# Kernel tuning notes

Measured on AMD Instinct MI355X. Metric: run time of the kernel, lower is better.

Reference implementation:

```python
import jax, jax.numpy as jnp
import numpy as np

B, T, I, H, O = 8192, 512, 4, 32, 4


def setup_inputs() -> dict:
    key = jax.random.key(0)
    ks = jax.random.split(key, 11)
    s = 1.0 / np.sqrt(H)  # PyTorch RNN init scale
    return {
        "X": jax.random.normal(ks[0], (B, T, I), dtype=jnp.float32),
        "W_ih0": jax.random.uniform(ks[1], (H, I), minval=-s, maxval=s, dtype=jnp.float32),
        "W_hh0": jax.random.uniform(ks[2], (H, H), minval=-s, maxval=s, dtype=jnp.float32),
        "b_ih0": jax.random.uniform(ks[3], (H,), minval=-s, maxval=s, dtype=jnp.float32),
        "b_hh0": jax.random.uniform(ks[4], (H,), minval=-s, maxval=s, dtype=jnp.float32),
        "W_ih1": jax.random.uniform(ks[5], (H, H), minval=-s, maxval=s, dtype=jnp.float32),
        "W_hh1": jax.random.uniform(ks[6], (H, H), minval=-s, maxval=s, dtype=jnp.float32),
        "b_ih1": jax.random.uniform(ks[7], (H,), minval=-s, maxval=s, dtype=jnp.float32),
        "b_hh1": jax.random.uniform(ks[8], (H,), minval=-s, maxval=s, dtype=jnp.float32),
        "W_ll": jax.random.uniform(ks[9], (O, H), minval=-s, maxval=s, dtype=jnp.float32),
        "b_ll": jax.random.uniform(ks[10], (O,), minval=-s, maxval=s, dtype=jnp.float32),
    }


def reference(X, W_ih0, W_hh0, b_ih0, b_hh0, W_ih1, W_hh1, b_ih1, b_hh1, W_ll, b_ll):
    # 2-layer tanh RNN (batch_first), zero initial hidden state, then Linear head.
    b0 = b_ih0 + b_hh0
    b1 = b_ih1 + b_hh1
    Bsz = X.shape[0]
    Hdim = W_hh0.shape[0]
    h_init = (jnp.zeros((Bsz, Hdim), X.dtype), jnp.zeros((Bsz, Hdim), X.dtype))

    def step(h, x_t):
        h0, h1 = h
        h0 = jnp.tanh(x_t @ W_ih0.T + h0 @ W_hh0.T + b0)
        h1 = jnp.tanh(h0 @ W_ih1.T + h1 @ W_hh1.T + b1)
        return (h0, h1), h1

    xs = jnp.swapaxes(X, 0, 1)  # [T, B, I]
    _, ys = jax.lax.scan(step, h_init, xs)  # ys: [T, B, H]
    out = ys @ W_ll.T + b_ll  # [T, B, O]
    out = jnp.swapaxes(out, 0, 1)  # [B, T, O]
    return out.reshape(out.shape[0], -1)  # [B, T*O]
```

## Files before the change

### kernel.cpp

```cpp
#include <hip/hip_runtime.h>
#include <cstddef>
#include <cstdint>

constexpr int kB = 8192, kT = 512, kI = 4, kH = 32, kO = 4;

typedef _Float16 f16x8 __attribute__((ext_vector_type(8)));
typedef float    f32x4 __attribute__((ext_vector_type(4)));

#define MFMA(a, b, c) __builtin_amdgcn_mfma_f32_16x16x32_f16((a), (b), (c), 0, 0, 0)

__device__ __forceinline__ void bar_lds() {
    asm volatile("s_waitcnt lgkmcnt(0)" ::: "memory");
    __builtin_amdgcn_s_barrier();
    __builtin_amdgcn_sched_barrier(0);
}

__device__ __forceinline__ float fast_tanh(float x) {
    float e = __builtin_amdgcn_exp2f(x * 2.8853900817779268f);
    return 1.0f - 2.0f * __builtin_amdgcn_rcpf(e + 1.0f);
}

__device__ __forceinline__ float4 ld4(const float* p) { return *(const float4*)p; }

__device__ __forceinline__ f16x8 pack_frag(float4 lo, float4 hi) {
    f16x8 r;
    r[0] = (_Float16)lo.x; r[1] = (_Float16)lo.y;
    r[2] = (_Float16)lo.z; r[3] = (_Float16)lo.w;
    r[4] = (_Float16)hi.x; r[5] = (_Float16)hi.y;
    r[6] = (_Float16)hi.z; r[7] = (_Float16)hi.w;
    return r;
}

__device__ __forceinline__ f16x8 pack_state(f32x4 a, f32x4 b) {
    union { f16x8 v; uint32_t u[4]; } r;
    r.u[0] = __builtin_bit_cast(uint32_t, __builtin_amdgcn_cvt_pkrtz(a[0], a[1]));
    r.u[1] = __builtin_bit_cast(uint32_t, __builtin_amdgcn_cvt_pkrtz(a[2], a[3]));
    r.u[2] = __builtin_bit_cast(uint32_t, __builtin_amdgcn_cvt_pkrtz(b[0], b[1]));
    r.u[3] = __builtin_bit_cast(uint32_t, __builtin_amdgcn_cvt_pkrtz(b[2], b[3]));
    return r.v;
}

__device__ __forceinline__ f16x8 bxpack(float4 xn, bool g0) {
    union { f16x8 v; uint32_t u[4]; } bx;
    bx.u[0] = g0 ? __builtin_bit_cast(uint32_t, __builtin_amdgcn_cvt_pkrtz(xn.x, xn.y)) : 0u;
    bx.u[1] = g0 ? __builtin_bit_cast(uint32_t, __builtin_amdgcn_cvt_pkrtz(xn.z, xn.w)) : 0u;
    bx.u[2] = 0u; bx.u[3] = 0u;
    return bx.v;
}

__global__ __launch_bounds__(256, 2) void rnn2_roles(
    const float* __restrict__ X,
    const float* __restrict__ W_ih0, const float* __restrict__ W_hh0,
    const float* __restrict__ b_ih0, const float* __restrict__ b_hh0,
    const float* __restrict__ W_ih1, const float* __restrict__ W_hh1,
    const float* __restrict__ b_ih1, const float* __restrict__ b_hh1,
    const float* __restrict__ W_ll, const float* __restrict__ b_ll,
    float* __restrict__ out)
{
    const int  tid = threadIdx.x;
    const int  wid = tid >> 6;
    const int  l   = tid & 63;
    const int  c   = l & 15;
    const int  g   = l >> 4;
    const bool g0  = (g == 0);
    const int  b   = blockIdx.x * 16 + c;
    const int  k0  = 4 * g;
    const int  role = wid ^ (((blockIdx.x >> 3) & 1) << 1);

    __shared__ f32x4 xcring[2][2][64];
    __shared__ uint4 h0ring[2][64];
    __shared__ uint4 h1ring[2][64];

    const float4 z4 = make_float4(0.f, 0.f, 0.f, 0.f);
    union { f16x8 v; uint32_t u[4]; } zz;
    zz.u[0] = zz.u[1] = zz.u[2] = zz.u[3] = 0u;

    if (role == 0) {
        const float* wp = W_hh0 + c * kH;
        const f16x8 A0 = pack_frag(ld4(wp + k0), ld4(wp + 16 + k0));
        wp = W_hh0 + (c + 16) * kH;
        const f16x8 A1 = pack_frag(ld4(wp + k0), ld4(wp + 16 + k0));
        f16x8 Bh0 = zz.v;
        f32x4 xcR0 = {0.f,0.f,0.f,0.f}, xcR1 = {0.f,0.f,0.f,0.f};

        for (int pb = 0; pb < 130; ++pb) {
#pragma unroll
            for (int u = 0; u < 4; ++u) {
                const int p = pb * 4 + u;
                f32x4 nx0, nx1;
                const bool rd = (p >= 1) & (p <= 512);
                const bool go = (p >= 2) & (p <= 513);
                if (rd) {
                    nx0 = xcring[(p - 1) & 1][0][l];
                    nx1 = xcring[(p - 1) & 1][1][l];
                }
                if (go) {
                    f32x4 a0 = MFMA(A0, Bh0, xcR0);
                    f32x4 a1 = MFMA(A1, Bh0, xcR1);
                    f32x4 t0, t1;
#pragma unroll
                    for (int r = 0; r < 4; ++r) { t0[r] = fast_tanh(a0[r]); t1[r] = fast_tanh(a1[r]); }
                    Bh0 = pack_state(t0, t1);
                    h0ring[p & 1][l] = __builtin_bit_cast(uint4, Bh0);
                }
                if (rd) { xcR0 = nx0; xcR1 = nx1; }
                bar_lds();
            }
        }
    } else if (role == 1) {
        const float* wp = W_ih1 + c * kH;
        const f16x8 I0 = pack_frag(ld4(wp + k0), ld4(wp + 16 + k0));
        wp = W_ih1 + (c + 16) * kH;
        const f16x8 I1 = pack_frag(ld4(wp + k0), ld4(wp + 16 + k0));
        wp = W_hh1 + c * kH;
        const f16x8 H0w = pack_frag(ld4(wp + k0), ld4(wp + 16 + k0));
        wp = W_hh1 + (c + 16) * kH;
        const f16x8 H1w = pack_frag(ld4(wp + k0), ld4(wp + 16 + k0));
        f32x4 bias1_0, bias1_1;
#pragma unroll
        for (int r = 0; r < 4; ++r) {
            bias1_0[r] = b_ih1[k0 + r]      + b_hh1[k0 + r];
            bias1_1[r] = b_ih1[16 + k0 + r] + b_hh1[16 + k0 + r];
        }
        f16x8 Bh1 = zz.v;
        f32x4 pB0 = {0.f,0.f,0.f,0.f}, pB1 = {0.f,0.f,0.f,0.f};

        for (int pb = 0; pb < 130; ++pb) {
#pragma unroll
            for (int u = 0; u < 4; ++u) {
                const int p = pb * 4 + u;
                f16x8 H;
                const bool rd = (p >= 3) & (p <= 514);
                const bool go = (p >= 4) & (p <= 515);
                if (rd) H = __builtin_bit_cast(f16x8, h0ring[(p - 3) & 1][l]);
                if (go) {
                    f32x4 q0 = MFMA(H0w, Bh1, pB0);
                    f32x4 q1 = MFMA(H1w, Bh1, pB1);
                    f32x4 t0, t1;
#pragma unroll
                    for (int r = 0; r < 4; ++r) { t0[r] = fast_tanh(q0[r]); t1[r] = fast_tanh(q1[r]); }
                    Bh1 = pack_state(t0, t1);
                    h1ring[p & 1][l] = __builtin_bit_cast(uint4, Bh1);
                }
                if (rd) {
                    pB0 = MFMA(I0, H, bias1_0);
                    pB1 = MFMA(I1, H, bias1_1);
                }
                bar_lds();
            }
        }
    } else if (role == 2) {
        const f16x8 W0 = pack_frag(g0 ? ld4(W_ih0 + c * kI) : z4, z4);
        const f16x8 W1 = pack_frag(g0 ? ld4(W_ih0 + (c + 16) * kI) : z4, z4);
        f32x4 bias0_0, bias0_1;
#pragma unroll
        for (int r = 0; r < 4; ++r) {
            bias0_0[r] = b_ih0[k0 + r]      + b_hh0[k0 + r];
            bias0_1[r] = b_ih0[16 + k0 + r] + b_hh0[16 + k0 + r];
        }
        const float* xp = X + (size_t)b * (kT * kI);
        float4 xbuf[4];
#pragma unroll
        for (int u = 0; u < 4; ++u) xbuf[u] = ld4(xp + u * kI);

        for (int pb = 0; pb < 130; ++pb) {
#pragma unroll
            for (int u = 0; u < 4; ++u) {
                const int p = pb * 4 + u;
                if (p < kT) {
                    f16x8 bx = bxpack(xbuf[u], g0);
                    f32x4 c0 = MFMA(W0, bx, bias0_0);
                    f32x4 c1 = MFMA(W1, bx, bias0_1);
                    xcring[p & 1][0][l] = c0;
                    xcring[p & 1][1][l] = c1;
                    int idx = p + 4; idx = idx < kT ? idx : (kT - 1);
                    xbuf[u] = ld4(xp + idx * kI);
                }
                bar_lds();
            }
        }
    } else {
        const f16x8 All = (c < kO)
            ? pack_frag(ld4(W_ll + c * kH + k0), ld4(W_ll + c * kH + 16 + k0))
            : pack_frag(z4, z4);
        f32x4 biasll;
#pragma unroll
        for (int r = 0; r < 4; ++r) biasll[r] = g0 ? b_ll[r] : 0.f;
        float* op = out + (size_t)b * (kT * kO);

        for (int pb = 0; pb < 130; ++pb) {
#pragma unroll
            for (int u = 0; u < 4; ++u) {
                const int p = pb * 4 + u;
                const bool go = (p >= 5) & (p <= 516);
                if (go) {
                    f16x8 H1 = __builtin_bit_cast(f16x8, h1ring[(p - 1) & 1][l]);
                    f32x4 o = MFMA(All, H1, biasll);
                    if (g0) *(float4*)(op + (size_t)(p - 5) * kO) =
                        make_float4(o[0], o[1], o[2], o[3]);
                }
                bar_lds();
            }
        }
    }
}

extern "C" void kernel_launch(void* const* d_in, const int* in_sizes, int n_in,
                              void* d_out, int out_size, void* d_ws, size_t ws_size,
                              hipStream_t stream) {
    const float* X     = (const float*)d_in[0];
    const float* W_ih0 = (const float*)d_in[1];
    const float* W_hh0 = (const float*)d_in[2];
    const float* b_ih0 = (const float*)d_in[3];
    const float* b_hh0 = (const float*)d_in[4];
    const float* W_ih1 = (const float*)d_in[5];
    const float* W_hh1 = (const float*)d_in[6];
    const float* b_ih1 = (const float*)d_in[7];
    const float* b_hh1 = (const float*)d_in[8];
    const float* W_ll  = (const float*)d_in[9];
    const float* b_ll  = (const float*)d_in[10];
    float* out = (float*)d_out;

    rnn2_roles<<<dim3(kB / 16), dim3(256), 0, stream>>>(
        X, W_ih0, W_hh0, b_ih0, b_hh0, W_ih1, W_hh1, b_ih1, b_hh1, W_ll, b_ll, out);
}
```

Baseline: 148.8 us.

## Prescale RNN weights for exp2 tanh and peel role loops with 4-deep rings

Folds the 2/ln2 factor of the exp2-based tanh into the layer weights and biases at load time. This removes one multiply per tanh on the serial recurrence, and the final step becomes an fma. Each role's time loop is split into an unrolled prologue, a predicate-free steady-state loop and an unrolled epilogue. The LDS rings grow from 2 to 4 slots, and the role-to-wave swizzle now alternates per block. The per-step barrier is kept, so the gains come from shorter dependent chains and less predication. The cost is slightly more LDS and code size, plus the rounding error of scaling weights before the fp16 conversion.

```diff
diff --git a/kernel.cpp b/kernel.cpp
--- a/kernel.cpp
+++ b/kernel.cpp
@@ -8,6 +8,8 @@
 typedef float    f32x4 __attribute__((ext_vector_type(4)));
 
 #define MFMA(a, b, c) __builtin_amdgcn_mfma_f32_16x16x32_f16((a), (b), (c), 0, 0, 0)
+
+constexpr float kPre = 2.8853900817779268f;
 
 __device__ __forceinline__ void bar_lds() {
     asm volatile("s_waitcnt lgkmcnt(0)" ::: "memory");
@@ -15,12 +17,16 @@
     __builtin_amdgcn_sched_barrier(0);
 }
 
-__device__ __forceinline__ float fast_tanh(float x) {
-    float e = __builtin_amdgcn_exp2f(x * 2.8853900817779268f);
-    return 1.0f - 2.0f * __builtin_amdgcn_rcpf(e + 1.0f);
+__device__ __forceinline__ float fast_tanh_pre(float xp) {
+    float e = __builtin_amdgcn_exp2f(xp);
+    return fmaf(-2.0f, __builtin_amdgcn_rcpf(e + 1.0f), 1.0f);
 }
 
 __device__ __forceinline__ float4 ld4(const float* p) { return *(const float4*)p; }
+
+__device__ __forceinline__ float4 scl4(float4 v, float s) {
+    return make_float4(v.x * s, v.y * s, v.z * s, v.w * s);
+}
 
 __device__ __forceinline__ f16x8 pack_frag(float4 lo, float4 hi) {
     f16x8 r;
@@ -40,15 +46,15 @@
     return r.v;
 }
 
-__device__ __forceinline__ f16x8 bxpack(float4 xn, bool g0) {
+__device__ __forceinline__ f16x8 bxpack(float4 xn) {
     union { f16x8 v; uint32_t u[4]; } bx;
-    bx.u[0] = g0 ? __builtin_bit_cast(uint32_t, __builtin_amdgcn_cvt_pkrtz(xn.x, xn.y)) : 0u;
-    bx.u[1] = g0 ? __builtin_bit_cast(uint32_t, __builtin_amdgcn_cvt_pkrtz(xn.z, xn.w)) : 0u;
+    bx.u[0] = __builtin_bit_cast(uint32_t, __builtin_amdgcn_cvt_pkrtz(xn.x, xn.y));
+    bx.u[1] = __builtin_bit_cast(uint32_t, __builtin_amdgcn_cvt_pkrtz(xn.z, xn.w));
     bx.u[2] = 0u; bx.u[3] = 0u;
     return bx.v;
 }
 
-__global__ __launch_bounds__(256, 2) void rnn2_roles(
+__global__ __launch_bounds__(256, 2) void rnn2_pipe4(
     const float* __restrict__ X,
     const float* __restrict__ W_ih0, const float* __restrict__ W_hh0,
     const float* __restrict__ b_ih0, const float* __restrict__ b_hh0,
@@ -65,11 +71,11 @@
     const bool g0  = (g == 0);
     const int  b   = blockIdx.x * 16 + c;
     const int  k0  = 4 * g;
-    const int  role = wid ^ (((blockIdx.x >> 3) & 1) << 1);
-
-    __shared__ f32x4 xcring[2][2][64];
-    __shared__ uint4 h0ring[2][64];
-    __shared__ uint4 h1ring[2][64];
+    const int  role = wid ^ ((blockIdx.x & 1) << 1);
+
+    __shared__ f32x4 xcring[4][2][64];
+    __shared__ uint4 h0ring[4][64];
+    __shared__ uint4 h1ring[4][64];
 
     const float4 z4 = make_float4(0.f, 0.f, 0.f, 0.f);
     union { f16x8 v; uint32_t u[4]; } zz;
@@ -77,108 +83,116 @@
 
     if (role == 0) {
         const float* wp = W_hh0 + c * kH;
-        const f16x8 A0 = pack_frag(ld4(wp + k0), ld4(wp + 16 + k0));
+        const f16x8 A0w = pack_frag(scl4(ld4(wp + k0), kPre), scl4(ld4(wp + 16 + k0), kPre));
         wp = W_hh0 + (c + 16) * kH;
-        const f16x8 A1 = pack_frag(ld4(wp + k0), ld4(wp + 16 + k0));
+        const f16x8 A1w = pack_frag(scl4(ld4(wp + k0), kPre), scl4(ld4(wp + 16 + k0), kPre));
         f16x8 Bh0 = zz.v;
         f32x4 xcR0 = {0.f,0.f,0.f,0.f}, xcR1 = {0.f,0.f,0.f,0.f};
 
-        for (int pb = 0; pb < 130; ++pb) {
-#pragma unroll
-            for (int u = 0; u < 4; ++u) {
-                const int p = pb * 4 + u;
-                f32x4 nx0, nx1;
-                const bool rd = (p >= 1) & (p <= 512);
-                const bool go = (p >= 2) & (p <= 513);
-                if (rd) {
-                    nx0 = xcring[(p - 1) & 1][0][l];
-                    nx1 = xcring[(p - 1) & 1][1][l];
-                }
-                if (go) {
-                    f32x4 a0 = MFMA(A0, Bh0, xcR0);
-                    f32x4 a1 = MFMA(A1, Bh0, xcR1);
-                    f32x4 t0, t1;
-#pragma unroll
-                    for (int r = 0; r < 4; ++r) { t0[r] = fast_tanh(a0[r]); t1[r] = fast_tanh(a1[r]); }
-                    Bh0 = pack_state(t0, t1);
-                    h0ring[p & 1][l] = __builtin_bit_cast(uint4, Bh0);
-                }
-                if (rd) { xcR0 = nx0; xcR1 = nx1; }
-                bar_lds();
-            }
-        }
+        auto ph = [&](int p, bool rd, bool go) {
+            f32x4 nx0, nx1;
+            if (rd) {
+                nx0 = xcring[(p - 1) & 3][0][l];
+                nx1 = xcring[(p - 1) & 3][1][l];
+            }
+            if (go) {
+                f32x4 a0 = MFMA(A0w, Bh0, xcR0);
+                f32x4 a1 = MFMA(A1w, Bh0, xcR1);
+                f32x4 t0, t1;
+#pragma unroll
+                for (int r = 0; r < 4; ++r) { t0[r] = fast_tanh_pre(a0[r]); t1[r] = fast_tanh_pre(a1[r]); }
+                Bh0 = pack_state(t0, t1);
+                h0ring[(p - 2) & 3][l] = __builtin_bit_cast(uint4, Bh0);
+            }
+            if (rd) { xcR0 = nx0; xcR1 = nx1; }
+        };
+
+#pragma unroll
+        for (int p = 0; p < 8; ++p) { ph(p, p >= 1, p >= 2); bar_lds(); }
+        for (int pb = 0; pb < 124; ++pb) {
+#pragma unroll
+            for (int u = 0; u < 4; ++u) { ph(8 + pb * 4 + u, true, true); bar_lds(); }
+        }
+#pragma unroll
+        for (int p = 504; p < 520; ++p) { ph(p, p <= 512, p <= 513); bar_lds(); }
     } else if (role == 1) {
         const float* wp = W_ih1 + c * kH;
-        const f16x8 I0 = pack_frag(ld4(wp + k0), ld4(wp + 16 + k0));
+        const f16x8 I0 = pack_frag(scl4(ld4(wp + k0), kPre), scl4(ld4(wp + 16 + k0), kPre));
         wp = W_ih1 + (c + 16) * kH;
-        const f16x8 I1 = pack_frag(ld4(wp + k0), ld4(wp + 16 + k0));
+        const f16x8 I1 = pack_frag(scl4(ld4(wp + k0), kPre), scl4(ld4(wp + 16 + k0), kPre));
         wp = W_hh1 + c * kH;
-        const f16x8 H0w = pack_frag(ld4(wp + k0), ld4(wp + 16 + k0));
+        const f16x8 H0w = pack_frag(scl4(ld4(wp + k0), kPre), scl4(ld4(wp + 16 + k0), kPre));
         wp = W_hh1 + (c + 16) * kH;
-        const f16x8 H1w = pack_frag(ld4(wp + k0), ld4(wp + 16 + k0));
+        const f16x8 H1w = pack_frag(scl4(ld4(wp + k0), kPre), scl4(ld4(wp + 16 + k0), kPre));
         f32x4 bias1_0, bias1_1;
 #pragma unroll
         for (int r = 0; r < 4; ++r) {
-            bias1_0[r] = b_ih1[k0 + r]      + b_hh1[k0 + r];
-            bias1_1[r] = b_ih1[16 + k0 + r] + b_hh1[16 + k0 + r];
+            bias1_0[r] = (b_ih1[k0 + r]      + b_hh1[k0 + r])      * kPre;
+            bias1_1[r] = (b_ih1[16 + k0 + r] + b_hh1[16 + k0 + r]) * kPre;
         }
         f16x8 Bh1 = zz.v;
         f32x4 pB0 = {0.f,0.f,0.f,0.f}, pB1 = {0.f,0.f,0.f,0.f};
 
-        for (int pb = 0; pb < 130; ++pb) {
-#pragma unroll
-            for (int u = 0; u < 4; ++u) {
-                const int p = pb * 4 + u;
-                f16x8 H;
-                const bool rd = (p >= 3) & (p <= 514);
-                const bool go = (p >= 4) & (p <= 515);
-                if (rd) H = __builtin_bit_cast(f16x8, h0ring[(p - 3) & 1][l]);
-                if (go) {
-                    f32x4 q0 = MFMA(H0w, Bh1, pB0);
-                    f32x4 q1 = MFMA(H1w, Bh1, pB1);
-                    f32x4 t0, t1;
-#pragma unroll
-                    for (int r = 0; r < 4; ++r) { t0[r] = fast_tanh(q0[r]); t1[r] = fast_tanh(q1[r]); }
-                    Bh1 = pack_state(t0, t1);
-                    h1ring[p & 1][l] = __builtin_bit_cast(uint4, Bh1);
-                }
-                if (rd) {
-                    pB0 = MFMA(I0, H, bias1_0);
-                    pB1 = MFMA(I1, H, bias1_1);
-                }
-                bar_lds();
-            }
-        }
+        auto ph = [&](int p, bool rd, bool go) {
+            f16x8 Hn;
+            if (rd) Hn = __builtin_bit_cast(f16x8, h0ring[(p - 3) & 3][l]);
+            if (go) {
+                f32x4 q0 = MFMA(H0w, Bh1, pB0);
+                f32x4 q1 = MFMA(H1w, Bh1, pB1);
+                f32x4 t0, t1;
+#pragma unroll
+                for (int r = 0; r < 4; ++r) { t0[r] = fast_tanh_pre(q0[r]); t1[r] = fast_tanh_pre(q1[r]); }
+                Bh1 = pack_state(t0, t1);
+                h1ring[(p - 4) & 3][l] = __builtin_bit_cast(uint4, Bh1);
+            }
+            if (rd) {
+                pB0 = MFMA(I0, Hn, bias1_0);
+                pB1 = MFMA(I1, Hn, bias1_1);
+            }
+        };
+
+#pragma unroll
+        for (int p = 0; p < 8; ++p) { ph(p, p >= 3, p >= 4); bar_lds(); }
+        for (int pb = 0; pb < 124; ++pb) {
+#pragma unroll
+            for (int u = 0; u < 4; ++u) { ph(8 + pb * 4 + u, true, true); bar_lds(); }
+        }
+#pragma unroll
+        for (int p = 504; p < 520; ++p) { ph(p, p <= 514, p <= 515); bar_lds(); }
     } else if (role == 2) {
-        const f16x8 W0 = pack_frag(g0 ? ld4(W_ih0 + c * kI) : z4, z4);
-        const f16x8 W1 = pack_frag(g0 ? ld4(W_ih0 + (c + 16) * kI) : z4, z4);
+        const f16x8 W0 = pack_frag(g0 ? scl4(ld4(W_ih0 + c * kI), kPre) : z4, z4);
+        const f16x8 W1 = pack_frag(g0 ? scl4(ld4(W_ih0 + (c + 16) * kI), kPre) : z4, z4);
         f32x4 bias0_0, bias0_1;
 #pragma unroll
         for (int r = 0; r < 4; ++r) {
-            bias0_0[r] = b_ih0[k0 + r]      + b_hh0[k0 + r];
-            bias0_1[r] = b_ih0[16 + k0 + r] + b_hh0[16 + k0 + r];
+            bias0_0[r] = (b_ih0[k0 + r]      + b_hh0[k0 + r])      * kPre;
+            bias0_1[r] = (b_ih0[16 + k0 + r] + b_hh0[16 + k0 + r]) * kPre;
         }
         const float* xp = X + (size_t)b * (kT * kI);
         float4 xbuf[4];
 #pragma unroll
         for (int u = 0; u < 4; ++u) xbuf[u] = ld4(xp + u * kI);
 
-        for (int pb = 0; pb < 130; ++pb) {
-#pragma unroll
-            for (int u = 0; u < 4; ++u) {
-                const int p = pb * 4 + u;
-                if (p < kT) {
-                    f16x8 bx = bxpack(xbuf[u], g0);
-                    f32x4 c0 = MFMA(W0, bx, bias0_0);
-                    f32x4 c1 = MFMA(W1, bx, bias0_1);
-                    xcring[p & 1][0][l] = c0;
-                    xcring[p & 1][1][l] = c1;
-                    int idx = p + 4; idx = idx < kT ? idx : (kT - 1);
-                    xbuf[u] = ld4(xp + idx * kI);
-                }
-                bar_lds();
-            }
-        }
+        auto ph = [&](int p, bool go, int xi) {
+            if (go) {
+                f16x8 bx = bxpack(xbuf[xi]);
+                f32x4 c0 = MFMA(W0, bx, bias0_0);
+                f32x4 c1 = MFMA(W1, bx, bias0_1);
+                xcring[xi][0][l] = c0;
+                xcring[xi][1][l] = c1;
+                int idx = p + 4; idx = idx < kT ? idx : (kT - 1);
+                xbuf[xi] = ld4(xp + idx * kI);
+            }
+        };
+
+#pragma unroll
+        for (int p = 0; p < 8; ++p) { ph(p, true, p & 3); bar_lds(); }
+        for (int pb = 0; pb < 124; ++pb) {
+#pragma unroll
+            for (int u = 0; u < 4; ++u) { ph(8 + pb * 4 + u, true, u); bar_lds(); }
+        }
+#pragma unroll
+        for (int p = 504; p < 520; ++p) { ph(p, p <= 511, p & 3); bar_lds(); }
     } else {
         const f16x8 All = (c < kO)
             ? pack_frag(ld4(W_ll + c * kH + k0), ld4(W_ll + c * kH + 16 + k0))
@@ -188,20 +202,23 @@
         for (int r = 0; r < 4; ++r) biasll[r] = g0 ? b_ll[r] : 0.f;
         float* op = out + (size_t)b * (kT * kO);
 
-        for (int pb = 0; pb < 130; ++pb) {
-#pragma unroll
-            for (int u = 0; u < 4; ++u) {
-                const int p = pb * 4 + u;
-                const bool go = (p >= 5) & (p <= 516);
-                if (go) {
-                    f16x8 H1 = __builtin_bit_cast(f16x8, h1ring[(p - 1) & 1][l]);
-                    f32x4 o = MFMA(All, H1, biasll);
-                    if (g0) *(float4*)(op + (size_t)(p - 5) * kO) =
-                        make_float4(o[0], o[1], o[2], o[3]);
-                }
-                bar_lds();
-            }
-        }
+        auto ph = [&](int p, bool go) {
+            if (go) {
+                f16x8 H1 = __builtin_bit_cast(f16x8, h1ring[(p - 5) & 3][l]);
+                f32x4 o = MFMA(All, H1, biasll);
+                if (g0) *(float4*)(op + (size_t)(p - 5) * kO) =
+                    make_float4(o[0], o[1], o[2], o[3]);
+            }
+        };
+
+#pragma unroll
+        for (int p = 0; p < 8; ++p) { ph(p, p >= 5); bar_lds(); }
+        for (int pb = 0; pb < 124; ++pb) {
+#pragma unroll
+            for (int u = 0; u < 4; ++u) { ph(8 + pb * 4 + u, true); bar_lds(); }
+        }
+#pragma unroll
+        for (int p = 504; p < 520; ++p) { ph(p, p <= 516); bar_lds(); }
     }
 }
 
@@ -221,6 +238,6 @@
     const float* b_ll  = (const float*)d_in[10];
     float* out = (float*)d_out;
 
-    rnn2_roles<<<dim3(kB / 16), dim3(256), 0, stream>>>(
+    rnn2_pipe4<<<dim3(kB / 16), dim3(256), 0, stream>>>(
         X, W_ih0, W_hh0, b_ih0, b_hh0, W_ih1, W_hh1, b_ih1, b_hh1, W_ll, b_ll, out);
 }
```

After: 145.4 us. 1.02x faster.
